# Performance work log

Hardware: AMD Instinct MI355X
Metric: run time of the kernel (lower is better)

## Reference

```python
import jax, jax.numpy as jnp
import numpy as np

NUM_BLOCKS = 8
SPARSITY = 0.01
HARD_FRAC = 1.0
HSF = 1  # hidden_size_factor
SCALE = 0.02


def setup_inputs() -> dict:
    key = jax.random.key(0)
    ks = jax.random.split(key, 5)
    B, H, W, C = 4, 90, 180, 768
    nb, bs = NUM_BLOCKS, C // NUM_BLOCKS
    x = jax.random.normal(ks[0], (B, H, W, C), jnp.float32)
    w1 = SCALE * jax.random.normal(ks[1], (2, nb, bs, bs * HSF), jnp.float32)
    b1 = SCALE * jax.random.normal(ks[2], (2, nb, bs * HSF), jnp.float32)
    w2 = SCALE * jax.random.normal(ks[3], (2, nb, bs * HSF, bs), jnp.float32)
    b2 = SCALE * jax.random.normal(ks[4], (2, nb, bs), jnp.float32)
    return {"x": x, "w1": w1, "b1": b1, "w2": w2, "b2": b2}


def _softshrink(v, lam):
    # torch.F.softshrink: v-lam if v>lam, v+lam if v<-lam, else 0
    return jnp.sign(v) * jnp.maximum(jnp.abs(v) - lam, 0.0)


def reference(x, w1, b1, w2, b2):
    bias = x
    B, H, W, C = x.shape
    nb, bs = NUM_BLOCKS, C // NUM_BLOCKS
    Wh = W // 2 + 1
    xf = jnp.fft.rfft2(x.astype(jnp.float32), axes=(1, 2), norm='ortho')  # [B,H,Wh,C] c64
    xf = xf.reshape(B, H, Wh, nb, bs)
    total_modes = H // 2 + 1
    kept_modes = int(total_modes * HARD_FRAC)
    r0 = total_modes - kept_modes
    r1 = min(total_modes + kept_modes, H)   # torch slicing clips at H
    c1 = min(kept_modes, Wh)
    xs = xf[:, r0:r1, :c1]                  # [B,hk,wk,nb,bs]
    xr, xi = jnp.real(xs), jnp.imag(xs)
    mm = lambda a, w: jnp.einsum('bhwni,nio->bhwno', a, w)
    # complex 2-layer block-diagonal MLP in split real/imag form
    o1r = jax.nn.relu(mm(xr, w1[0]) - mm(xi, w1[1]) + b1[0])
    o1i = jax.nn.relu(mm(xi, w1[0]) + mm(xr, w1[1]) + b1[1])
    o2r = _softshrink(mm(o1r, w2[0]) - mm(o1i, w2[1]) + b2[0], SPARSITY)
    o2i = _softshrink(mm(o1i, w2[0]) + mm(o1r, w2[1]) + b2[1], SPARSITY)
    z = jnp.zeros((B, H, Wh, nb, bs), jnp.complex64)
    z = z.at[:, r0:r1, :c1].set((o2r + 1j * o2i).astype(jnp.complex64))
    y = jnp.fft.irfft2(z.reshape(B, H, Wh, C), s=(H, W), axes=(1, 2), norm='ortho')
    return y.astype(x.dtype) + bias
```

## Files before the change

### kernel.cpp

```cpp
#include <hip/hip_runtime.h>
#include <math.h>

typedef __attribute__((ext_vector_type(8))) short short8;
typedef __attribute__((ext_vector_type(4))) float f32x4;

#define MFMA16 __builtin_amdgcn_mfma_f32_16x16x32_bf16

namespace {

constexpr float kI180 = 0.07453559924999299f;
constexpr float kI90  = 0.10540925533894598f;
constexpr float kTwoPi = 6.283185307179586f;

__device__ inline unsigned short f2b(float f) {
  unsigned u = __builtin_bit_cast(unsigned, f);
  u += 0x7fffu + ((u >> 16) & 1u);
  return (unsigned short)(u >> 16);
}

__global__ void prep_k(short* cTw, short* cThf, short* cThi, short* cW1,
                       short* cW2, short* cTwi, float* fB1, float* fB2,
                       const float* __restrict__ w1, const float* __restrict__ b1,
                       const float* __restrict__ w2, const float* __restrict__ b2) {
  int gid = blockIdx.x * blockDim.x + threadIdx.x;
  int gs = gridDim.x * blockDim.x;
  for (int i = gid; i < 96 * 192; i += gs) {
    int n = i / 192, k = i % 192;
    int ri = n / 48, wp = n % 48;
    float v = 0.f;
    if (wp < 46 && k < 180) {
      int r = (k * wp) % 180;
      float s, c;
      sincosf(kTwoPi * (float)r / 180.f, &s, &c);
      v = (ri == 0) ? c * kI180 : -s * kI180;
    }
    cTw[i] = (short)f2b(v);
  }
  for (int i = gid; i < 192 * 192; i += gs) {
    int n = i / 192, k = i % 192;
    int rj = n / 96, hp = n % 96;
    int ri = k / 96, h = k % 96;
    float vf = 0.f, vi = 0.f;
    if (hp < 90 && h < 90) {
      int r = (h * hp) % 90;
      float s, c;
      sincosf(kTwoPi * (float)r / 90.f, &s, &c);
      c *= kI90; s *= kI90;
      vf = (rj == 0) ? ((ri == 0) ? c : s) : ((ri == 0) ? -s : c);
      vi = (rj == 0) ? ((ri == 0) ? c : -s) : ((ri == 0) ? s : c);
    }
    cThf[i] = (short)f2b(vf);
    cThi[i] = (short)f2b(vi);
  }
  for (int i = gid; i < 8 * 192 * 192; i += gs) {
    int n = i / 36864, r2 = i % 36864;
    int j = r2 / 192, k = r2 % 192;
    int rj = j / 96, o = j % 96;
    int ri = k / 96, ci = k % 96;
    {
      float W0 = w1[((size_t)(n * 96 + ci)) * 96 + o];
      float W1v = w1[((size_t)((8 + n) * 96 + ci)) * 96 + o];
      float v = (rj == 0) ? ((ri == 0) ? W0 : -W1v) : ((ri == 0) ? W1v : W0);
      cW1[i] = (short)f2b(v);
    }
    {
      float W0 = w2[((size_t)(n * 96 + ci)) * 96 + o];
      float W1v = w2[((size_t)((8 + n) * 96 + ci)) * 96 + o];
      float v = (rj == 0) ? ((ri == 0) ? W0 : -W1v) : ((ri == 0) ? W1v : W0);
      cW2[i] = (short)f2b(v);
    }
  }
  for (int i = gid; i < 192 * 96; i += gs) {
    int n = i / 96, k = i % 96;
    int ri = k / 48, wp = k % 48;
    float v = 0.f;
    if (n < 180 && wp < 46) {
      int r = (n * wp) % 180;
      float s, c;
      sincosf(kTwoPi * (float)r / 180.f, &s, &c);
      if (ri == 0) v = ((wp == 0) ? 1.f : 2.f) * c * kI180;
      else v = (wp == 0) ? 0.f : -2.f * s * kI180;
    }
    cTwi[i] = (short)f2b(v);
  }
  for (int i = gid; i < 8 * 192; i += gs) {
    int n = i / 192, j = i % 192;
    int rj = j / 96, o = j % 96;
    fB1[i] = b1[(size_t)(rj * 8 + n) * 96 + o];
    fB2[i] = b2[(size_t)(rj * 8 + n) * 96 + o];
  }
}

__global__ __launch_bounds__(256, 4) void s1_k(const float* __restrict__ x,
                                               const short* __restrict__ cTw,
                                               short* __restrict__ X1a) {
  __shared__ short Bl[96 * 200];
  int t = threadIdx.x;
  int bh = blockIdx.x;
  int c0 = blockIdx.y * 64;
  {
    short8 tb[9];
#pragma unroll
    for (int i = 0; i < 9; ++i) {
      int q = t + i * 256;
      int r = q / 24, s = q % 24;
      tb[i] = *(const short8*)&cTw[r * 192 + s * 8];
    }
#pragma unroll
    for (int i = 0; i < 9; ++i) {
      int q = t + i * 256;
      int r = q / 24, s = q % 24;
      *(short8*)&Bl[r * 200 + s * 8] = tb[i];
    }
  }
  int lane = t & 63, wv = t >> 6, ln = lane & 15, qd = lane >> 4;
  int c = c0 + wv * 16 + ln;
  const float* xc = x + (size_t)bh * 180 * 768 + c;
  float xv[48];
#pragma unroll
  for (int kc = 0; kc < 6; ++kc) {
#pragma unroll
    for (int j = 0; j < 8; ++j) {
      int w = kc * 32 + qd * 8 + j;
      int wl = w < 180 ? w : 0;
      xv[kc * 8 + j] = xc[(size_t)wl * 768];
    }
  }
  short8 a[6];
#pragma unroll
  for (int kc = 0; kc < 6; ++kc) {
#pragma unroll
    for (int j = 0; j < 8; ++j) {
      int w = kc * 32 + qd * 8 + j;
      float v = (w < 180) ? xv[kc * 8 + j] : 0.f;
      a[kc][j] = (short)f2b(v);
    }
  }
  __syncthreads();
  f32x4 z = {0.f, 0.f, 0.f, 0.f};
  f32x4 acc[6];
#pragma unroll
  for (int i = 0; i < 6; ++i) acc[i] = z;
#pragma unroll
  for (int kc = 0; kc < 6; ++kc) {
    int ko = kc * 32 + qd * 8;
#pragma unroll
    for (int nf = 0; nf < 6; ++nf) {
      short8 bv = *(const short8*)&Bl[(nf * 16 + ln) * 200 + ko];
      acc[nf] = MFMA16(a[kc], bv, acc[nf], 0, 0, 0);
    }
  }
  short* dst = X1a + (size_t)bh * 96 * 768;
  int cbase = c0 + wv * 16 + qd * 4;
#pragma unroll
  for (int nf = 0; nf < 6; ++nf) {
    int n = nf * 16 + ln;
    short4 v;
    v.x = (short)f2b(acc[nf][0]);
    v.y = (short)f2b(acc[nf][1]);
    v.z = (short)f2b(acc[nf][2]);
    v.w = (short)f2b(acc[nf][3]);
    *(short4*)&dst[(size_t)n * 768 + cbase] = v;
  }
}

__global__ __launch_bounds__(256) void t1_k(const short* __restrict__ X1a,
                                            short* __restrict__ X1b) {
  __shared__ short L[64 * 104];
  unsigned* Ld = (unsigned*)L;
  int t = threadIdx.x;
  int gx = blockIdx.x;
  int c0 = blockIdx.y * 64;
  int b = gx / 92, r = gx % 92;
  int ri = r / 46, wp = r % 46;
  const short* src = X1a + ((size_t)(b * 90) * 96 + ri * 48 + wp) * 768 + c0;
  short8 r0a[2], r1a[2];
#pragma unroll
  for (int i = 0; i < 2; ++i) {
    int q = t + i * 256;
    int ql = q < 360 ? q : 0;
    int seg = ql & 7, hp = ql >> 3;
    int h0 = hp * 2;
    r0a[i] = *(const short8*)&src[(size_t)h0 * 73728 + seg * 8];
    r1a[i] = *(const short8*)&src[(size_t)(h0 + 1) * 73728 + seg * 8];
  }
#pragma unroll
  for (int i = 0; i < 2; ++i) {
    int q = t + i * 256;
    if (q < 360) {
      int seg = q & 7, hp = q >> 3;
#pragma unroll
      for (int j = 0; j < 8; ++j) {
        int cch = seg * 8 + j;
        Ld[cch * 52 + hp] = (unsigned)(unsigned short)r0a[i][j] |
                            ((unsigned)(unsigned short)r1a[i][j] << 16);
      }
    }
  }
  for (int q = t; q < 64 * 3; q += 256) {
    int cch = q / 3, hp = 45 + q % 3;
    Ld[cch * 52 + hp] = 0u;
  }
  __syncthreads();
  short* dst = X1b + (size_t)b * 35328 * 192 + ((size_t)wp * 768 + c0) * 192 + ri * 96;
  for (int q = t; q < 64 * 12; q += 256) {
    int cch = q / 12, seg = q % 12;
    short8 v = *(const short8*)&L[cch * 104 + seg * 8];
    *(short8*)&dst[(size_t)cch * 192 + seg * 8] = v;
  }
}

__global__ __launch_bounds__(256, 4) void s24_k(const short* __restrict__ Asrc,
                                                const short* __restrict__ Bsrc,
                                                short* __restrict__ dst) {
  __shared__ short Bl[96 * 200];
  int t = threadIdx.x;
  int mt = blockIdx.x, nh = blockIdx.y, b = blockIdx.z;
  {
    short8 tb[9];
#pragma unroll
    for (int i = 0; i < 9; ++i) {
      int q = t + i * 256;
      int r = q / 24, s = q % 24;
      tb[i] = *(const short8*)&Bsrc[(size_t)(nh * 96 + r) * 192 + s * 8];
    }
#pragma unroll
    for (int i = 0; i < 9; ++i) {
      int q = t + i * 256;
      int r = q / 24, s = q % 24;
      *(short8*)&Bl[r * 200 + s * 8] = tb[i];
    }
  }
  int lane = t & 63, wv = t >> 6, ln = lane & 15, qd = lane >> 4;
  const short* Ab = Asrc + ((size_t)b * 35328 + (size_t)mt * 64 + wv * 16 + ln) * 192;
  short8 a[6];
#pragma unroll
  for (int kc = 0; kc < 6; ++kc) a[kc] = *(const short8*)&Ab[kc * 32 + qd * 8];
  __syncthreads();
  f32x4 z = {0.f, 0.f, 0.f, 0.f};
  f32x4 acc[6];
#pragma unroll
  for (int i = 0; i < 6; ++i) acc[i] = z;
#pragma unroll
  for (int kc = 0; kc < 6; ++kc) {
    int ko = kc * 32 + qd * 8;
#pragma unroll
    for (int nf = 0; nf < 6; ++nf) {
      short8 bv = *(const short8*)&Bl[(nf * 16 + ln) * 200 + ko];
      acc[nf] = MFMA16(a[kc], bv, acc[nf], 0, 0, 0);
    }
  }
  size_t m0 = (size_t)mt * 64 + wv * 16 + qd * 4;
  short* db = dst + (size_t)b * 192 * 35328;
#pragma unroll
  for (int nf = 0; nf < 6; ++nf) {
    int n = nh * 96 + nf * 16 + ln;
    short4 v;
    v.x = (short)f2b(acc[nf][0]);
    v.y = (short)f2b(acc[nf][1]);
    v.z = (short)f2b(acc[nf][2]);
    v.w = (short)f2b(acc[nf][3]);
    *(short4*)&db[(size_t)n * 35328 + m0] = v;
  }
}

__global__ __launch_bounds__(256, 4) void s3a_k(const short* __restrict__ X2,
                                                const short* __restrict__ cW1,
                                                const float* __restrict__ fB1,
                                                short* __restrict__ O1) {
  __shared__ short Sh[96 * 200];
  int t = threadIdx.x;
  int mt = blockIdx.x;
  int n = blockIdx.y >> 1, nh = blockIdx.y & 1;
  {
    const short* Bsrc = cW1 + (size_t)n * 36864;
    short8 tb[9];
#pragma unroll
    for (int i = 0; i < 9; ++i) {
      int q = t + i * 256;
      int r = q / 24, s = q % 24;
      tb[i] = *(const short8*)&Bsrc[(size_t)(nh * 96 + r) * 192 + s * 8];
    }
#pragma unroll
    for (int i = 0; i < 9; ++i) {
      int q = t + i * 256;
      int r = q / 24, s = q % 24;
      *(short8*)&Sh[r * 200 + s * 8] = tb[i];
    }
  }
  int lane = t & 63, wv = t >> 6, ln = lane & 15, qd = lane >> 4;
  int p = mt * 64 + wv * 16 + ln;
  if (p > 16559) p = 16559;
  int pb = p / 4140, rem = p % 4140;
  int hp = rem / 46, wp = rem % 46;
  const short* Ap = X2 + ((size_t)pb * 192 + hp) * 35328 + (size_t)wp * 768 + n * 96;
  short8 a[6];
#pragma unroll
  for (int kc = 0; kc < 6; ++kc) {
    int ko = kc * 32 + qd * 8;
    int ri = kc / 3;
    int kl = ko - ri * 96;
    a[kc] = *(const short8*)&Ap[(size_t)ri * 96 * 35328 + kl];
  }
  __syncthreads();
  f32x4 z = {0.f, 0.f, 0.f, 0.f};
  f32x4 acc[6];
#pragma unroll
  for (int i = 0; i < 6; ++i) acc[i] = z;
#pragma unroll
  for (int kc = 0; kc < 6; ++kc) {
    int ko = kc * 32 + qd * 8;
#pragma unroll
    for (int nf = 0; nf < 6; ++nf) {
      short8 bv = *(const short8*)&Sh[(nf * 16 + ln) * 200 + ko];
      acc[nf] = MFMA16(a[kc], bv, acc[nf], 0, 0, 0);
    }
  }
  __syncthreads();
#pragma unroll
  for (int nf = 0; nf < 6; ++nf) {
    float bias = fB1[n * 192 + nh * 96 + nf * 16 + ln];
#pragma unroll
    for (int r = 0; r < 4; ++r) {
      float v = acc[nf][r] + bias;
      v = v > 0.f ? v : 0.f;
      Sh[(wv * 16 + qd * 4 + r) * 104 + nf * 16 + ln] = (short)f2b(v);
    }
  }
  __syncthreads();
  for (int q = t; q < 64 * 12; q += 256) {
    int pr = q / 12, seg = q % 12;
    int pp = mt * 64 + pr;
    if (pp < 16560) {
      *(short8*)&O1[((size_t)n * 16576 + pp) * 192 + nh * 96 + seg * 8] =
          *(const short8*)&Sh[pr * 104 + seg * 8];
    }
  }
}

__global__ __launch_bounds__(256, 4) void s3b_k(const short* __restrict__ O1,
                                                const short* __restrict__ cW2,
                                                const float* __restrict__ fB2,
                                                short* __restrict__ O2) {
  __shared__ short Bl[96 * 200];
  int t = threadIdx.x;
  int mt = blockIdx.x;
  int n = blockIdx.y >> 1, nh = blockIdx.y & 1;
  {
    const short* Bsrc = cW2 + (size_t)n * 36864;
    short8 tb[9];
#pragma unroll
    for (int i = 0; i < 9; ++i) {
      int q = t + i * 256;
      int r = q / 24, s = q % 24;
      tb[i] = *(const short8*)&Bsrc[(size_t)(nh * 96 + r) * 192 + s * 8];
    }
#pragma unroll
    for (int i = 0; i < 9; ++i) {
      int q = t + i * 256;
      int r = q / 24, s = q % 24;
      *(short8*)&Bl[r * 200 + s * 8] = tb[i];
    }
  }
  int lane = t & 63, wv = t >> 6, ln = lane & 15, qd = lane >> 4;
  int p = mt * 64 + wv * 16 + ln;
  if (p > 16559) p = 16559;
  const short* Ab = O1 + ((size_t)n * 16576 + p) * 192;
  short8 a[6];
#pragma unroll
  for (int kc = 0; kc < 6; ++kc) a[kc] = *(const short8*)&Ab[kc * 32 + qd * 8];
  __syncthreads();
  f32x4 z = {0.f, 0.f, 0.f, 0.f};
  f32x4 acc[6];
#pragma unroll
  for (int i = 0; i < 6; ++i) acc[i] = z;
#pragma unroll
  for (int kc = 0; kc < 6; ++kc) {
    int ko = kc * 32 + qd * 8;
#pragma unroll
    for (int nf = 0; nf < 6; ++nf) {
      short8 bv = *(const short8*)&Bl[(nf * 16 + ln) * 200 + ko];
      acc[nf] = MFMA16(a[kc], bv, acc[nf], 0, 0, 0);
    }
  }
  size_t p0 = (size_t)mt * 64 + wv * 16 + qd * 4;
  if (p0 < 16560) {
#pragma unroll
    for (int nf = 0; nf < 6; ++nf) {
      int j = nh * 96 + nf * 16 + ln;
      float bias = fB2[n * 192 + j];
      short4 v;
      float s0;
      s0 = acc[nf][0] + bias; s0 = fabsf(s0) > 0.01f ? copysignf(fabsf(s0) - 0.01f, s0) : 0.f; v.x = (short)f2b(s0);
      s0 = acc[nf][1] + bias; s0 = fabsf(s0) > 0.01f ? copysignf(fabsf(s0) - 0.01f, s0) : 0.f; v.y = (short)f2b(s0);
      s0 = acc[nf][2] + bias; s0 = fabsf(s0) > 0.01f ? copysignf(fabsf(s0) - 0.01f, s0) : 0.f; v.z = (short)f2b(s0);
      s0 = acc[nf][3] + bias; s0 = fabsf(s0) > 0.01f ? copysignf(fabsf(s0) - 0.01f, s0) : 0.f; v.w = (short)f2b(s0);
      *(short4*)&O2[((size_t)n * 192 + j) * 16576 + p0] = v;
    }
  }
}

__global__ __launch_bounds__(256) void t2_k(const short* __restrict__ O2,
                                            short* __restrict__ X3) {
  __shared__ short L[16 * 1488];
  int t = threadIdx.x;
  int gx = blockIdx.x;
  int ht = gx % 3; gx /= 3;
  int ot = gx % 6; gx /= 6;
  int rj = gx % 2; gx /= 2;
  int n = gx % 8;
  int b = gx / 8;
  int h0 = ht * 32;
  int nh = min(32, 90 - h0);
  int o0 = ot * 16;
  int posbase = (b * 90 + h0) * 46;
  int pa = posbase & ~7;
  int d = posbase - pa;
  int vlen = d + 46 * nh;
  int segs = (vlen + 7) / 8;
  for (int q = t; q < 16 * 186; q += 256) {
    int orl = q / 186, seg = q % 186;
    if (seg < segs) {
      short8 v = *(const short8*)&O2[((size_t)n * 192 + rj * 96 + o0 + orl) * 16576 +
                                     pa + seg * 8];
      int base = seg * 8;
      if (base >= d && base + 8 <= vlen) {
        *(short8*)&L[orl * 1488 + base] = v;
      } else {
#pragma unroll
        for (int i = 0; i < 8; ++i) {
          int col = base + i;
          L[orl * 1488 + col] = (col >= d && col < vlen) ? v[i] : (short)0;
        }
      }
    } else {
      short8 zz = {0, 0, 0, 0, 0, 0, 0, 0};
      *(short8*)&L[orl * 1488 + seg * 8] = zz;
    }
  }
  __syncthreads();
  short* dst = X3 + (size_t)b * 35328 * 192;
  for (int q = t; q < 46 * 64; q += 256) {
    int wp = q >> 6;
    int rem = q & 63;
    int orl = rem >> 2, seg = rem & 3;
    short8 v;
#pragma unroll
    for (int i = 0; i < 8; ++i) {
      int hrel = seg * 8 + i;
      v[i] = L[orl * 1488 + d + hrel * 46 + wp];
    }
    *(short8*)&dst[((size_t)wp * 768 + n * 96 + o0 + orl) * 192 + rj * 96 + h0 +
                   seg * 8] = v;
  }
}

__global__ __launch_bounds__(256, 3) void s5_k(const short* __restrict__ X4,
                                               const short* __restrict__ cTwi,
                                               const float* __restrict__ x,
                                               float* __restrict__ out) {
  __shared__ short Bl[192 * 104];
  __shared__ short Al[64 * 104];
  int t = threadIdx.x;
  int bh = blockIdx.x;
  int c0 = blockIdx.y * 64;
  int b = bh / 90, h = bh % 90;
  {
    short8 tb[9];
#pragma unroll
    for (int i = 0; i < 9; ++i) {
      int q = t + i * 256;
      int r = q / 12, s = q % 12;
      tb[i] = *(const short8*)&cTwi[r * 96 + s * 8];
    }
#pragma unroll
    for (int i = 0; i < 9; ++i) {
      int q = t + i * 256;
      int r = q / 12, s = q % 12;
      *(short8*)&Bl[r * 104 + s * 8] = tb[i];
    }
  }
  {
    short8 ta[3];
    int kk[3], cc[3];
#pragma unroll
    for (int i = 0; i < 3; ++i) {
      int q = t + i * 256;
      int cs = q & 7, k = q >> 3;
      int ri = k / 48, wp = k % 48;
      if (wp > 45) wp = 45;
      ta[i] = *(const short8*)&X4[((size_t)b * 192 + ri * 96 + h) * 35328 +
                                  (size_t)wp * 768 + c0 + cs * 8];
      kk[i] = k; cc[i] = cs;
    }
#pragma unroll
    for (int i = 0; i < 3; ++i) {
#pragma unroll
      for (int j = 0; j < 8; ++j) Al[(cc[i] * 8 + j) * 104 + kk[i]] = ta[i][j];
    }
  }
  __syncthreads();
  int lane = t & 63, wv = t >> 6, ln = lane & 15, qd = lane >> 4;
  f32x4 z = {0.f, 0.f, 0.f, 0.f};
  f32x4 acc[12];
#pragma unroll
  for (int i = 0; i < 12; ++i) acc[i] = z;
  int arow = (wv * 16 + ln) * 104;
#pragma unroll
  for (int kc = 0; kc < 3; ++kc) {
    int ko = kc * 32 + qd * 8;
    short8 av = *(const short8*)&Al[arow + ko];
#pragma unroll
    for (int nf = 0; nf < 12; ++nf) {
      short8 bv = *(const short8*)&Bl[(nf * 16 + ln) * 104 + ko];
      acc[nf] = MFMA16(av, bv, acc[nf], 0, 0, 0);
    }
  }
  int cb = c0 + wv * 16 + qd * 4;
  const float* xr = x + (size_t)bh * 180 * 768;
  float* ob = out + (size_t)bh * 180 * 768;
  float4 xv[12];
#pragma unroll
  for (int nf = 0; nf < 12; ++nf) {
    int w = nf * 16 + ln;
    int wl = w < 180 ? w : 0;
    xv[nf] = *(const float4*)&xr[(size_t)wl * 768 + cb];
  }
#pragma unroll
  for (int nf = 0; nf < 12; ++nf) {
    int w = nf * 16 + ln;
    if (w < 180) {
      float4 o;
      o.x = acc[nf][0] + xv[nf].x;
      o.y = acc[nf][1] + xv[nf].y;
      o.z = acc[nf][2] + xv[nf].z;
      o.w = acc[nf][3] + xv[nf].w;
      *(float4*)&ob[(size_t)w * 768 + cb] = o;
    }
  }
}

}

extern "C" void kernel_launch(void* const* d_in, const int* in_sizes, int n_in,
                              void* d_out, int out_size, void* d_ws, size_t ws_size,
                              hipStream_t stream) {
  const float* x = (const float*)d_in[0];
  const float* w1 = (const float*)d_in[1];
  const float* b1 = (const float*)d_in[2];
  const float* w2 = (const float*)d_in[3];
  const float* b2 = (const float*)d_in[4];
  float* out = (float*)d_out;

  size_t off = 0;
  auto carve = [&](size_t bytes) -> char* {
    char* p = (char*)d_ws + off;
    off += (bytes + 255) & ~(size_t)255;
    return p;
  };
  short* cTw = (short*)carve(96 * 192 * 2);
  short* cThf = (short*)carve(192 * 192 * 2);
  short* cThi = (short*)carve(192 * 192 * 2);
  short* cW1 = (short*)carve(8 * 192 * 192 * 2);
  short* cW2 = (short*)carve(8 * 192 * 192 * 2);
  short* cTwi = (short*)carve(192 * 96 * 2);
  float* fB1 = (float*)carve(8 * 192 * 4);
  float* fB2 = (float*)carve(8 * 192 * 4);
  const size_t SLOT = 27131904;
  short* slotA = (short*)carve(SLOT * 2);
  short* slotB = (short*)carve(SLOT * 2);
  short* X1a = slotA;
  short* X1b = slotB;
  short* X2 = slotA;
  short* O1 = slotB;
  short* O2 = slotA;
  short* X3 = slotB;
  short* X4 = slotA;

  prep_k<<<512, 256, 0, stream>>>(cTw, cThf, cThi, cW1, cW2, cTwi, fB1, fB2,
                                  w1, b1, w2, b2);
  s1_k<<<dim3(360, 12), 256, 0, stream>>>(x, cTw, X1a);
  t1_k<<<dim3(368, 12), 256, 0, stream>>>(X1a, X1b);
  s24_k<<<dim3(552, 2, 4), 256, 0, stream>>>(X1b, cThf, X2);
  s3a_k<<<dim3(259, 16), 256, 0, stream>>>(X2, cW1, fB1, O1);
  s3b_k<<<dim3(259, 16), 256, 0, stream>>>(O1, cW2, fB2, O2);
  t2_k<<<dim3(1152), 256, 0, stream>>>(O2, X3);
  s24_k<<<dim3(552, 2, 4), 256, 0, stream>>>(X3, cThi, X4);
  s5_k<<<dim3(360, 12), 256, 0, stream>>>(X4, cTwi, x, out);
}
```

Before: 613.9 us.

## Fuse spectral MLP layers, merge N-halves in GEMMs, restructure weight prep

Fuses the two MLP GEMM kernels into one s3_k that keeps the layer-1 activations in LDS and feeds them straight into layer 2. This removes the O1 round trip through global memory and one launch. The s24 kernels now compute both 96-column halves per block, loading the A tile once and restaging B twice. s5 halves its LDS for B by staging it in two passes, letting occupancy rise to 4. Weight prep is rewritten to transpose through shared memory with coalesced loads on a smaller grid. The cost is extra barriers and B restaging inside each block, plus fewer, larger blocks.

```diff
diff --git a/kernel.cpp b/kernel.cpp
--- a/kernel.cpp
+++ b/kernel.cpp
@@ -18,12 +18,103 @@
   return (unsigned short)(u >> 16);
 }
 
-__global__ void prep_k(short* cTw, short* cThf, short* cThi, short* cW1,
-                       short* cW2, short* cTwi, float* fB1, float* fB2,
+__device__ __forceinline__ void stage_b(short* Bl, const short* src, int t) {
+  short8 tb[9];
+#pragma unroll
+  for (int i = 0; i < 9; ++i) {
+    int q = t + i * 256;
+    int r = q / 24, s = q % 24;
+    tb[i] = *(const short8*)&src[(size_t)r * 192 + s * 8];
+  }
+#pragma unroll
+  for (int i = 0; i < 9; ++i) {
+    int q = t + i * 256;
+    int r = q / 24, s = q % 24;
+    *(short8*)&Bl[r * 200 + s * 8] = tb[i];
+  }
+}
+
+__device__ __forceinline__ void stage_b96(short* Bl, const short* src, int t) {
+  short8 tb[5];
+#pragma unroll
+  for (int i = 0; i < 5; ++i) {
+    int q = t + i * 256;
+    int ql = q < 1152 ? q : 0;
+    int r = ql / 12, s = ql % 12;
+    tb[i] = *(const short8*)&src[r * 96 + s * 8];
+  }
+#pragma unroll
+  for (int i = 0; i < 5; ++i) {
+    int q = t + i * 256;
+    if (q < 1152) {
+      int r = q / 12, s = q % 12;
+      *(short8*)&Bl[r * 104 + s * 8] = tb[i];
+    }
+  }
+}
+
+__device__ __forceinline__ void mfma6(f32x4* acc, const short8* a,
+                                      const short* Bl, int ln, int qd) {
+  f32x4 z = {0.f, 0.f, 0.f, 0.f};
+#pragma unroll
+  for (int i = 0; i < 6; ++i) acc[i] = z;
+#pragma unroll
+  for (int kc = 0; kc < 6; ++kc) {
+    int ko = kc * 32 + qd * 8;
+#pragma unroll
+    for (int nf = 0; nf < 6; ++nf) {
+      short8 bv = *(const short8*)&Bl[(nf * 16 + ln) * 200 + ko];
+      acc[nf] = MFMA16(a[kc], bv, acc[nf], 0, 0, 0);
+    }
+  }
+}
+
+__global__ __launch_bounds__(256) void prep_k(short* cTw, short* cThf, short* cThi,
+                       short* cW1, short* cW2, short* cTwi, float* fB1, float* fB2,
                        const float* __restrict__ w1, const float* __restrict__ b1,
                        const float* __restrict__ w2, const float* __restrict__ b2) {
-  int gid = blockIdx.x * blockDim.x + threadIdx.x;
-  int gs = gridDim.x * blockDim.x;
+  int bx = blockIdx.x, t = threadIdx.x;
+  if (bx < 16) {
+    __shared__ short Wt[2 * 96 * 104];
+    int n = bx & 7;
+    const float* src = (bx < 8) ? w1 : w2;
+    short* dstm = (bx < 8) ? cW1 : cW2;
+#pragma unroll
+    for (int pl = 0; pl < 2; ++pl) {
+      const float* p = src + (size_t)(pl * 8 + n) * 9216;
+      float4 tv[9];
+#pragma unroll
+      for (int i = 0; i < 9; ++i) tv[i] = *(const float4*)&p[(t + i * 256) * 4];
+#pragma unroll
+      for (int i = 0; i < 9; ++i) {
+        int idx = t + i * 256;
+        int ci = idx / 24, oq = idx % 24;
+        short* wp_ = &Wt[pl * 96 * 104];
+        wp_[(oq * 4 + 0) * 104 + ci] = (short)f2b(tv[i].x);
+        wp_[(oq * 4 + 1) * 104 + ci] = (short)f2b(tv[i].y);
+        wp_[(oq * 4 + 2) * 104 + ci] = (short)f2b(tv[i].z);
+        wp_[(oq * 4 + 3) * 104 + ci] = (short)f2b(tv[i].w);
+      }
+    }
+    __syncthreads();
+#pragma unroll
+    for (int u = 0; u < 18; ++u) {
+      int idx = t + u * 256;
+      int jrow = idx / 24, sq = idx % 24;
+      int rj = jrow / 96, o = jrow % 96;
+      int ri = sq / 12, ciq = sq % 12;
+      int pl = rj ^ ri;
+      short8 v = *(const short8*)&Wt[pl * 96 * 104 + o * 104 + ciq * 8];
+      if (rj == 0 && ri == 1) {
+#pragma unroll
+        for (int j = 0; j < 8; ++j) v[j] = (short)(v[j] ^ (short)0x8000);
+      }
+      *(short8*)&dstm[(size_t)n * 36864 + (size_t)jrow * 192 + sq * 8] = v;
+    }
+    return;
+  }
+  int gid = (bx - 16) * 256 + t;
+  const int gs = 8 * 256;
   for (int i = gid; i < 96 * 192; i += gs) {
     int n = i / 192, k = i % 192;
     int ri = n / 48, wp = n % 48;
@@ -52,24 +143,6 @@
     cThf[i] = (short)f2b(vf);
     cThi[i] = (short)f2b(vi);
   }
-  for (int i = gid; i < 8 * 192 * 192; i += gs) {
-    int n = i / 36864, r2 = i % 36864;
-    int j = r2 / 192, k = r2 % 192;
-    int rj = j / 96, o = j % 96;
-    int ri = k / 96, ci = k % 96;
-    {
-      float W0 = w1[((size_t)(n * 96 + ci)) * 96 + o];
-      float W1v = w1[((size_t)((8 + n) * 96 + ci)) * 96 + o];
-      float v = (rj == 0) ? ((ri == 0) ? W0 : -W1v) : ((ri == 0) ? W1v : W0);
-      cW1[i] = (short)f2b(v);
-    }
-    {
-      float W0 = w2[((size_t)(n * 96 + ci)) * 96 + o];
-      float W1v = w2[((size_t)((8 + n) * 96 + ci)) * 96 + o];
-      float v = (rj == 0) ? ((ri == 0) ? W0 : -W1v) : ((ri == 0) ? W1v : W0);
-      cW2[i] = (short)f2b(v);
-    }
-  }
   for (int i = gid; i < 192 * 96; i += gs) {
     int n = i / 96, k = i % 96;
     int ri = k / 48, wp = k % 48;
@@ -98,21 +171,7 @@
   int t = threadIdx.x;
   int bh = blockIdx.x;
   int c0 = blockIdx.y * 64;
-  {
-    short8 tb[9];
-#pragma unroll
-    for (int i = 0; i < 9; ++i) {
-      int q = t + i * 256;
-      int r = q / 24, s = q % 24;
-      tb[i] = *(const short8*)&cTw[r * 192 + s * 8];
-    }
-#pragma unroll
-    for (int i = 0; i < 9; ++i) {
-      int q = t + i * 256;
-      int r = q / 24, s = q % 24;
-      *(short8*)&Bl[r * 200 + s * 8] = tb[i];
-    }
-  }
+  stage_b(Bl, cTw, t);
   int lane = t & 63, wv = t >> 6, ln = lane & 15, qd = lane >> 4;
   int c = c0 + wv * 16 + ln;
   const float* xc = x + (size_t)bh * 180 * 768 + c;
@@ -137,19 +196,8 @@
     }
   }
   __syncthreads();
-  f32x4 z = {0.f, 0.f, 0.f, 0.f};
   f32x4 acc[6];
-#pragma unroll
-  for (int i = 0; i < 6; ++i) acc[i] = z;
-#pragma unroll
-  for (int kc = 0; kc < 6; ++kc) {
-    int ko = kc * 32 + qd * 8;
-#pragma unroll
-    for (int nf = 0; nf < 6; ++nf) {
-      short8 bv = *(const short8*)&Bl[(nf * 16 + ln) * 200 + ko];
-      acc[nf] = MFMA16(a[kc], bv, acc[nf], 0, 0, 0);
-    }
-  }
+  mfma6(acc, a, Bl, ln, qd);
   short* dst = X1a + (size_t)bh * 96 * 768;
   int cbase = c0 + wv * 16 + qd * 4;
 #pragma unroll
@@ -215,46 +263,25 @@
                                                 short* __restrict__ dst) {
   __shared__ short Bl[96 * 200];
   int t = threadIdx.x;
-  int mt = blockIdx.x, nh = blockIdx.y, b = blockIdx.z;
-  {
-    short8 tb[9];
-#pragma unroll
-    for (int i = 0; i < 9; ++i) {
-      int q = t + i * 256;
-      int r = q / 24, s = q % 24;
-      tb[i] = *(const short8*)&Bsrc[(size_t)(nh * 96 + r) * 192 + s * 8];
-    }
-#pragma unroll
-    for (int i = 0; i < 9; ++i) {
-      int q = t + i * 256;
-      int r = q / 24, s = q % 24;
-      *(short8*)&Bl[r * 200 + s * 8] = tb[i];
-    }
-  }
+  int mt = blockIdx.x, b = blockIdx.y;
   int lane = t & 63, wv = t >> 6, ln = lane & 15, qd = lane >> 4;
   const short* Ab = Asrc + ((size_t)b * 35328 + (size_t)mt * 64 + wv * 16 + ln) * 192;
   short8 a[6];
 #pragma unroll
   for (int kc = 0; kc < 6; ++kc) a[kc] = *(const short8*)&Ab[kc * 32 + qd * 8];
-  __syncthreads();
-  f32x4 z = {0.f, 0.f, 0.f, 0.f};
-  f32x4 acc[6];
-#pragma unroll
-  for (int i = 0; i < 6; ++i) acc[i] = z;
-#pragma unroll
-  for (int kc = 0; kc < 6; ++kc) {
-    int ko = kc * 32 + qd * 8;
-#pragma unroll
-    for (int nf = 0; nf < 6; ++nf) {
-      short8 bv = *(const short8*)&Bl[(nf * 16 + ln) * 200 + ko];
-      acc[nf] = MFMA16(a[kc], bv, acc[nf], 0, 0, 0);
-    }
-  }
+  stage_b(Bl, Bsrc, t);
+  __syncthreads();
+  f32x4 acc[12];
+  mfma6(acc, a, Bl, ln, qd);
+  __syncthreads();
+  stage_b(Bl, Bsrc + 96 * 192, t);
+  __syncthreads();
+  mfma6(acc + 6, a, Bl, ln, qd);
   size_t m0 = (size_t)mt * 64 + wv * 16 + qd * 4;
   short* db = dst + (size_t)b * 192 * 35328;
 #pragma unroll
-  for (int nf = 0; nf < 6; ++nf) {
-    int n = nh * 96 + nf * 16 + ln;
+  for (int nf = 0; nf < 12; ++nf) {
+    int n = (nf >= 6 ? 96 : 0) + (nf % 6) * 16 + ln;
     short4 v;
     v.x = (short)f2b(acc[nf][0]);
     v.y = (short)f2b(acc[nf][1]);
@@ -264,30 +291,15 @@
   }
 }
 
-__global__ __launch_bounds__(256, 4) void s3a_k(const short* __restrict__ X2,
-                                                const short* __restrict__ cW1,
-                                                const float* __restrict__ fB1,
-                                                short* __restrict__ O1) {
-  __shared__ short Sh[96 * 200];
+__global__ __launch_bounds__(256, 4) void s3_k(const short* __restrict__ X2,
+                                               const short* __restrict__ cW1,
+                                               const short* __restrict__ cW2,
+                                               const float* __restrict__ fB1,
+                                               const float* __restrict__ fB2,
+                                               short* __restrict__ O2) {
+  __shared__ short Bl[96 * 200];
   int t = threadIdx.x;
-  int mt = blockIdx.x;
-  int n = blockIdx.y >> 1, nh = blockIdx.y & 1;
-  {
-    const short* Bsrc = cW1 + (size_t)n * 36864;
-    short8 tb[9];
-#pragma unroll
-    for (int i = 0; i < 9; ++i) {
-      int q = t + i * 256;
-      int r = q / 24, s = q % 24;
-      tb[i] = *(const short8*)&Bsrc[(size_t)(nh * 96 + r) * 192 + s * 8];
-    }
-#pragma unroll
-    for (int i = 0; i < 9; ++i) {
-      int q = t + i * 256;
-      int r = q / 24, s = q % 24;
-      *(short8*)&Sh[r * 200 + s * 8] = tb[i];
-    }
-  }
+  int mt = blockIdx.x, n = blockIdx.y;
   int lane = t & 63, wv = t >> 6, ln = lane & 15, qd = lane >> 4;
   int p = mt * 64 + wv * 16 + ln;
   if (p > 16559) p = 16559;
@@ -302,100 +314,61 @@
     int kl = ko - ri * 96;
     a[kc] = *(const short8*)&Ap[(size_t)ri * 96 * 35328 + kl];
   }
-  __syncthreads();
-  f32x4 z = {0.f, 0.f, 0.f, 0.f};
-  f32x4 acc[6];
-#pragma unroll
-  for (int i = 0; i < 6; ++i) acc[i] = z;
-#pragma unroll
-  for (int kc = 0; kc < 6; ++kc) {
-    int ko = kc * 32 + qd * 8;
-#pragma unroll
-    for (int nf = 0; nf < 6; ++nf) {
-      short8 bv = *(const short8*)&Sh[(nf * 16 + ln) * 200 + ko];
-      acc[nf] = MFMA16(a[kc], bv, acc[nf], 0, 0, 0);
-    }
-  }
+  const short* B1 = cW1 + (size_t)n * 36864;
+  const short* B2 = cW2 + (size_t)n * 36864;
+  stage_b(Bl, B1, t);
+  __syncthreads();
+  f32x4 acc0[6], acc1[6];
+  mfma6(acc0, a, Bl, ln, qd);
+  __syncthreads();
+  stage_b(Bl, B1 + 96 * 192, t);
+  __syncthreads();
+  mfma6(acc1, a, Bl, ln, qd);
   __syncthreads();
 #pragma unroll
   for (int nf = 0; nf < 6; ++nf) {
-    float bias = fB1[n * 192 + nh * 96 + nf * 16 + ln];
+    float b0 = fB1[n * 192 + nf * 16 + ln];
+    float b1v = fB1[n * 192 + 96 + nf * 16 + ln];
 #pragma unroll
     for (int r = 0; r < 4; ++r) {
-      float v = acc[nf][r] + bias;
-      v = v > 0.f ? v : 0.f;
-      Sh[(wv * 16 + qd * 4 + r) * 104 + nf * 16 + ln] = (short)f2b(v);
-    }
-  }
-  __syncthreads();
-  for (int q = t; q < 64 * 12; q += 256) {
-    int pr = q / 12, seg = q % 12;
-    int pp = mt * 64 + pr;
-    if (pp < 16560) {
-      *(short8*)&O1[((size_t)n * 16576 + pp) * 192 + nh * 96 + seg * 8] =
-          *(const short8*)&Sh[pr * 104 + seg * 8];
-    }
-  }
-}
-
-__global__ __launch_bounds__(256, 4) void s3b_k(const short* __restrict__ O1,
-                                                const short* __restrict__ cW2,
-                                                const float* __restrict__ fB2,
-                                                short* __restrict__ O2) {
-  __shared__ short Bl[96 * 200];
-  int t = threadIdx.x;
-  int mt = blockIdx.x;
-  int n = blockIdx.y >> 1, nh = blockIdx.y & 1;
-  {
-    const short* Bsrc = cW2 + (size_t)n * 36864;
-    short8 tb[9];
-#pragma unroll
-    for (int i = 0; i < 9; ++i) {
-      int q = t + i * 256;
-      int r = q / 24, s = q % 24;
-      tb[i] = *(const short8*)&Bsrc[(size_t)(nh * 96 + r) * 192 + s * 8];
-    }
-#pragma unroll
-    for (int i = 0; i < 9; ++i) {
-      int q = t + i * 256;
-      int r = q / 24, s = q % 24;
-      *(short8*)&Bl[r * 200 + s * 8] = tb[i];
-    }
-  }
-  int lane = t & 63, wv = t >> 6, ln = lane & 15, qd = lane >> 4;
-  int p = mt * 64 + wv * 16 + ln;
-  if (p > 16559) p = 16559;
-  const short* Ab = O1 + ((size_t)n * 16576 + p) * 192;
-  short8 a[6];
-#pragma unroll
-  for (int kc = 0; kc < 6; ++kc) a[kc] = *(const short8*)&Ab[kc * 32 + qd * 8];
-  __syncthreads();
-  f32x4 z = {0.f, 0.f, 0.f, 0.f};
-  f32x4 acc[6];
-#pragma unroll
-  for (int i = 0; i < 6; ++i) acc[i] = z;
-#pragma unroll
-  for (int kc = 0; kc < 6; ++kc) {
-    int ko = kc * 32 + qd * 8;
-#pragma unroll
-    for (int nf = 0; nf < 6; ++nf) {
-      short8 bv = *(const short8*)&Bl[(nf * 16 + ln) * 200 + ko];
-      acc[nf] = MFMA16(a[kc], bv, acc[nf], 0, 0, 0);
-    }
-  }
+      int row = wv * 16 + qd * 4 + r;
+      float v0 = acc0[nf][r] + b0;
+      float v1 = acc1[nf][r] + b1v;
+      v0 = v0 > 0.f ? v0 : 0.f;
+      v1 = v1 > 0.f ? v1 : 0.f;
+      Bl[row * 200 + nf * 16 + ln] = (short)f2b(v0);
+      Bl[row * 200 + 96 + nf * 16 + ln] = (short)f2b(v1);
+    }
+  }
+  __syncthreads();
+#pragma unroll
+  for (int kc = 0; kc < 6; ++kc)
+    a[kc] = *(const short8*)&Bl[(wv * 16 + ln) * 200 + kc * 32 + qd * 8];
+  __syncthreads();
+  stage_b(Bl, B2, t);
+  __syncthreads();
+  mfma6(acc0, a, Bl, ln, qd);
+  __syncthreads();
+  stage_b(Bl, B2 + 96 * 192, t);
+  __syncthreads();
+  mfma6(acc1, a, Bl, ln, qd);
   size_t p0 = (size_t)mt * 64 + wv * 16 + qd * 4;
   if (p0 < 16560) {
 #pragma unroll
-    for (int nf = 0; nf < 6; ++nf) {
-      int j = nh * 96 + nf * 16 + ln;
-      float bias = fB2[n * 192 + j];
-      short4 v;
-      float s0;
-      s0 = acc[nf][0] + bias; s0 = fabsf(s0) > 0.01f ? copysignf(fabsf(s0) - 0.01f, s0) : 0.f; v.x = (short)f2b(s0);
-      s0 = acc[nf][1] + bias; s0 = fabsf(s0) > 0.01f ? copysignf(fabsf(s0) - 0.01f, s0) : 0.f; v.y = (short)f2b(s0);
-      s0 = acc[nf][2] + bias; s0 = fabsf(s0) > 0.01f ? copysignf(fabsf(s0) - 0.01f, s0) : 0.f; v.z = (short)f2b(s0);
-      s0 = acc[nf][3] + bias; s0 = fabsf(s0) > 0.01f ? copysignf(fabsf(s0) - 0.01f, s0) : 0.f; v.w = (short)f2b(s0);
-      *(short4*)&O2[((size_t)n * 192 + j) * 16576 + p0] = v;
+    for (int half = 0; half < 2; ++half) {
+      f32x4* ac = half ? acc1 : acc0;
+#pragma unroll
+      for (int nf = 0; nf < 6; ++nf) {
+        int j = half * 96 + nf * 16 + ln;
+        float bias = fB2[n * 192 + j];
+        short4 v;
+        float s0;
+        s0 = ac[nf][0] + bias; s0 = fabsf(s0) > 0.01f ? copysignf(fabsf(s0) - 0.01f, s0) : 0.f; v.x = (short)f2b(s0);
+        s0 = ac[nf][1] + bias; s0 = fabsf(s0) > 0.01f ? copysignf(fabsf(s0) - 0.01f, s0) : 0.f; v.y = (short)f2b(s0);
+        s0 = ac[nf][2] + bias; s0 = fabsf(s0) > 0.01f ? copysignf(fabsf(s0) - 0.01f, s0) : 0.f; v.z = (short)f2b(s0);
+        s0 = ac[nf][3] + bias; s0 = fabsf(s0) > 0.01f ? copysignf(fabsf(s0) - 0.01f, s0) : 0.f; v.w = (short)f2b(s0);
+        *(short4*)&O2[((size_t)n * 192 + j) * 16576 + p0] = v;
+      }
     }
   }
 }
@@ -455,31 +428,16 @@
   }
 }
 
-__global__ __launch_bounds__(256, 3) void s5_k(const short* __restrict__ X4,
+__global__ __launch_bounds__(256, 4) void s5_k(const short* __restrict__ X4,
                                                const short* __restrict__ cTwi,
                                                const float* __restrict__ x,
                                                float* __restrict__ out) {
-  __shared__ short Bl[192 * 104];
+  __shared__ short Bl[96 * 104];
   __shared__ short Al[64 * 104];
   int t = threadIdx.x;
   int bh = blockIdx.x;
   int c0 = blockIdx.y * 64;
   int b = bh / 90, h = bh % 90;
-  {
-    short8 tb[9];
-#pragma unroll
-    for (int i = 0; i < 9; ++i) {
-      int q = t + i * 256;
-      int r = q / 12, s = q % 12;
-      tb[i] = *(const short8*)&cTwi[r * 96 + s * 8];
-    }
-#pragma unroll
-    for (int i = 0; i < 9; ++i) {
-      int q = t + i * 256;
-      int r = q / 12, s = q % 12;
-      *(short8*)&Bl[r * 104 + s * 8] = tb[i];
-    }
-  }
   {
     short8 ta[3];
     int kk[3], cc[3];
@@ -499,6 +457,7 @@
       for (int j = 0; j < 8; ++j) Al[(cc[i] * 8 + j) * 104 + kk[i]] = ta[i][j];
     }
   }
+  stage_b96(Bl, cTwi, t);
   __syncthreads();
   int lane = t & 63, wv = t >> 6, ln = lane & 15, qd = lane >> 4;
   f32x4 z = {0.f, 0.f, 0.f, 0.f};
@@ -511,31 +470,48 @@
     int ko = kc * 32 + qd * 8;
     short8 av = *(const short8*)&Al[arow + ko];
 #pragma unroll
-    for (int nf = 0; nf < 12; ++nf) {
+    for (int nf = 0; nf < 6; ++nf) {
       short8 bv = *(const short8*)&Bl[(nf * 16 + ln) * 104 + ko];
+      acc[nf] = MFMA16(av, bv, acc[nf], 0, 0, 0);
+    }
+  }
+  __syncthreads();
+  stage_b96(Bl, cTwi + 96 * 96, t);
+  __syncthreads();
+#pragma unroll
+  for (int kc = 0; kc < 3; ++kc) {
+    int ko = kc * 32 + qd * 8;
+    short8 av = *(const short8*)&Al[arow + ko];
+#pragma unroll
+    for (int nf = 6; nf < 12; ++nf) {
+      short8 bv = *(const short8*)&Bl[((nf - 6) * 16 + ln) * 104 + ko];
       acc[nf] = MFMA16(av, bv, acc[nf], 0, 0, 0);
     }
   }
   int cb = c0 + wv * 16 + qd * 4;
   const float* xr = x + (size_t)bh * 180 * 768;
   float* ob = out + (size_t)bh * 180 * 768;
-  float4 xv[12];
-#pragma unroll
-  for (int nf = 0; nf < 12; ++nf) {
-    int w = nf * 16 + ln;
-    int wl = w < 180 ? w : 0;
-    xv[nf] = *(const float4*)&xr[(size_t)wl * 768 + cb];
-  }
-#pragma unroll
-  for (int nf = 0; nf < 12; ++nf) {
-    int w = nf * 16 + ln;
-    if (w < 180) {
-      float4 o;
-      o.x = acc[nf][0] + xv[nf].x;
-      o.y = acc[nf][1] + xv[nf].y;
-      o.z = acc[nf][2] + xv[nf].z;
-      o.w = acc[nf][3] + xv[nf].w;
-      *(float4*)&ob[(size_t)w * 768 + cb] = o;
+#pragma unroll
+  for (int g = 0; g < 2; ++g) {
+    float4 xv[6];
+#pragma unroll
+    for (int u = 0; u < 6; ++u) {
+      int w = (g * 6 + u) * 16 + ln;
+      int wl = w < 180 ? w : 0;
+      xv[u] = *(const float4*)&xr[(size_t)wl * 768 + cb];
+    }
+#pragma unroll
+    for (int u = 0; u < 6; ++u) {
+      int nf = g * 6 + u;
+      int w = nf * 16 + ln;
+      if (w < 180) {
+        float4 o;
+        o.x = acc[nf][0] + xv[u].x;
+        o.y = acc[nf][1] + xv[u].y;
+        o.z = acc[nf][2] + xv[u].z;
+        o.w = acc[nf][3] + xv[u].w;
+        *(float4*)&ob[(size_t)w * 768 + cb] = o;
+      }
     }
   }
 }
@@ -572,19 +548,17 @@
   short* X1a = slotA;
   short* X1b = slotB;
   short* X2 = slotA;
-  short* O1 = slotB;
-  short* O2 = slotA;
-  short* X3 = slotB;
-  short* X4 = slotA;
-
-  prep_k<<<512, 256, 0, stream>>>(cTw, cThf, cThi, cW1, cW2, cTwi, fB1, fB2,
-                                  w1, b1, w2, b2);
+  short* O2 = slotB;
+  short* X3 = slotA;
+  short* X4 = slotB;
+
+  prep_k<<<24, 256, 0, stream>>>(cTw, cThf, cThi, cW1, cW2, cTwi, fB1, fB2,
+                                 w1, b1, w2, b2);
   s1_k<<<dim3(360, 12), 256, 0, stream>>>(x, cTw, X1a);
   t1_k<<<dim3(368, 12), 256, 0, stream>>>(X1a, X1b);
-  s24_k<<<dim3(552, 2, 4), 256, 0, stream>>>(X1b, cThf, X2);
-  s3a_k<<<dim3(259, 16), 256, 0, stream>>>(X2, cW1, fB1, O1);
-  s3b_k<<<dim3(259, 16), 256, 0, stream>>>(O1, cW2, fB2, O2);
+  s24_k<<<dim3(552, 4), 256, 0, stream>>>(X1b, cThf, X2);
+  s3_k<<<dim3(259, 8), 256, 0, stream>>>(X2, cW1, cW2, fB1, fB2, O2);
   t2_k<<<dim3(1152), 256, 0, stream>>>(O2, X3);
-  s24_k<<<dim3(552, 2, 4), 256, 0, stream>>>(X3, cThi, X4);
+  s24_k<<<dim3(552, 4), 256, 0, stream>>>(X3, cThi, X4);
   s5_k<<<dim3(360, 12), 256, 0, stream>>>(X4, cTwi, x, out);
 }
```

After: 595.2 us. 1.03x faster.
